# Kernel optimization log

Measured on AMD Instinct MI355X. Metric: run time of the kernel, lower is better.

## Reference

```python
import jax, jax.numpy as jnp
import numpy as np

DS = 8  # downsample_factor


def learned_upflow(flow, mask, ds=DS):
    """Convex-combination upsampling, faithful to Model.learned_upflow.

    flow: (n, 2, h, w)   coarse flow at 1/ds resolution
    mask: (n, 9*ds*ds, h, w)  raw (pre-softmax) convex weights
    returns: (n, 2, ds*h, ds*w)
    """
    n, _, h, w = flow.shape
    # mask.view(n, 1, 9, ds, ds, h, w); softmax over the 9 neighbor taps
    m = mask.reshape(n, 1, 9, ds, ds, h, w)
    m = jax.nn.softmax(m, axis=2)

    # F.unfold(ds*flow, [3,3], padding=1) -> 3x3 neighborhoods, row-major
    # kernel order (dy outer, dx inner), channel-major — matches the
    # subsequent view(n, 2, 9, 1, 1, h, w).
    fp = jnp.pad(ds * flow, ((0, 0), (0, 0), (1, 1), (1, 1)))
    patches = jnp.stack(
        [fp[:, :, dy:dy + h, dx:dx + w] for dy in range(3) for dx in range(3)],
        axis=2,
    )  # (n, 2, 9, h, w)

    up = jnp.sum(m * patches[:, :, :, None, None, :, :], axis=2)  # (n,2,ds,ds,h,w)
    # permute(0,1,4,2,5,3) then reshape -> (n, 2, ds*h, ds*w)
    up = up.transpose(0, 1, 4, 2, 5, 3)
    return up.reshape(n, 2, ds * h, ds * w)


def setup_inputs() -> dict:
    key = jax.random.key(0)
    k1, k2 = jax.random.split(key)
    n, h, w = 4, 136, 240
    flow = jax.random.normal(k1, (n, 2, h, w), dtype=jnp.float32)
    mask = jax.random.normal(k2, (n, 9 * DS * DS, h, w), dtype=jnp.float32)
    return {"flow": flow, "mask": mask}


def reference(flow, mask):
    return learned_upflow(flow, mask)
```

## Files before the change

kernel.cpp:

```cpp
#include <hip/hip_runtime.h>

#define HH 136
#define WW 240
#define HW (HH * WW)
#define DS 8
#define OW (DS * WW)
#define OH (DS * HH)
#define CROWS 12
#define NCH 6

typedef float vf4 __attribute__((ext_vector_type(4)));

__device__ __forceinline__ void gload_lds16(const float* g, float* l) {
  __builtin_amdgcn_global_load_lds(
      (const __attribute__((address_space(1))) void*)g,
      (__attribute__((address_space(3))) void*)l, 16, 0, 0);
}

__global__ __launch_bounds__(256, 7) void upflow_kernel(
    const float* __restrict__ flow,
    const float* __restrict__ mask,
    float* __restrict__ out) {
  __shared__ float lm[2][CROWS][WW];

  int h = blockIdx.x;
  int ni = blockIdx.y;
  int i = ni & 7;
  int n = ni >> 3;
  int tid = threadIdx.x;
  int wid = tid >> 6, lane = tid & 63;
  int px = tid;
  bool stager = lane < 60;

  const float* mrow = mask + ((size_t)n * 576 + i * 8) * HW + (size_t)h * WW;

  if (stager) {
#pragma unroll
    for (int t = 0; t < 3; ++t) {
      int rr = wid + 4 * t;
      gload_lds16(mrow + (size_t)((rr >> 3) * 64 + (rr & 7)) * HW + lane * 4,
                  &lm[0][rr][0]);
    }
  }

  float f0[9], f1[9];
  if (px < WW) {
    const float* fb0 = flow + (size_t)(n * 2 + 0) * HW;
    const float* fb1 = flow + (size_t)(n * 2 + 1) * HW;
#pragma unroll
    for (int dy = 0; dy < 3; ++dy) {
      int hh = h + dy - 1;
      bool rok = (hh >= 0) && (hh < HH);
#pragma unroll
      for (int dx = 0; dx < 3; ++dx) {
        int k = dy * 3 + dx;
        int cc = px + dx - 1;
        bool ok = rok && (cc >= 0) && (cc < WW);
        int idx = hh * WW + cc;
        f0[k] = ok ? 8.0f * fb0[idx] : 0.0f;
        f1[k] = ok ? 8.0f * fb1[idx] : 0.0f;
      }
    }
  }

  const float L2E = 1.4426950408889634f;
  float sj[8], d0j[8], d1j[8];
#pragma unroll
  for (int j = 0; j < 8; ++j) { sj[j] = 0.f; d0j[j] = 0.f; d1j[j] = 0.f; }

#pragma unroll
  for (int c = 0; c < NCH; ++c) {
    if (c + 1 < NCH) {
      if (stager) {
#pragma unroll
        for (int t = 0; t < 3; ++t) {
          int rr = wid + 4 * t;
          int g = (c + 1) * CROWS + rr;
          gload_lds16(
              mrow + (size_t)((g >> 3) * 64 + (g & 7)) * HW + lane * 4,
              &lm[(c + 1) & 1][rr][0]);
        }
      }
      asm volatile("s_waitcnt vmcnt(3)" ::: "memory");
    } else {
      asm volatile("s_waitcnt vmcnt(0)" ::: "memory");
    }
    __builtin_amdgcn_s_barrier();
    asm volatile("" ::: "memory");

    if (px < WW) {
#pragma unroll
      for (int rr = 0; rr < CROWS; ++rr) {
        const int g = c * CROWS + rr;
        const int k = g >> 3, j = g & 7;
        float e = exp2f(lm[c & 1][rr][px] * L2E);
        sj[j] += e;
        d0j[j] += e * f0[k];
        d1j[j] += e * f1[k];
      }
    }

    if (c + 1 < NCH) {
      asm volatile("" ::: "memory");
      __builtin_amdgcn_s_barrier();
      asm volatile("" ::: "memory");
    }
  }

  if (px < WW) {
    size_t ob0 =
        ((size_t)(n * 2 + 0) * OH + (size_t)(h * 8 + i)) * (size_t)OW + px * 8;
    size_t ob1 = ob0 + (size_t)OH * OW;
    float r0 = 1.0f / sj[0], r1 = 1.0f / sj[1], r2 = 1.0f / sj[2],
          r3 = 1.0f / sj[3], r4 = 1.0f / sj[4], r5 = 1.0f / sj[5],
          r6 = 1.0f / sj[6], r7 = 1.0f / sj[7];
    vf4 a = {d0j[0] * r0, d0j[1] * r1, d0j[2] * r2, d0j[3] * r3};
    vf4 b = {d0j[4] * r4, d0j[5] * r5, d0j[6] * r6, d0j[7] * r7};
    vf4 c = {d1j[0] * r0, d1j[1] * r1, d1j[2] * r2, d1j[3] * r3};
    vf4 d = {d1j[4] * r4, d1j[5] * r5, d1j[6] * r6, d1j[7] * r7};
    *(vf4*)(out + ob0) = a;
    *(vf4*)(out + ob0 + 4) = b;
    *(vf4*)(out + ob1) = c;
    *(vf4*)(out + ob1 + 4) = d;
  }
}

extern "C" void kernel_launch(void* const* d_in, const int* in_sizes, int n_in,
                              void* d_out, int out_size, void* d_ws, size_t ws_size,
                              hipStream_t stream) {
  const float* flow = (const float*)d_in[0];
  const float* mask = (const float*)d_in[1];
  float* out = (float*)d_out;
  dim3 grid(HH, 32);
  upflow_kernel<<<grid, 256, 0, stream>>>(flow, mask, out);
}
```

Baseline: 74.66 us.

## Use per-wave private LDS triple buffering and drop block barriers

Each wave now stages only the 60-pixel slice of mask rows it consumes into its own LDS region, so no cross-wave s_barrier is needed. Staging uses 15 lanes issuing 16-byte direct-to-LDS loads, with chunks of 9 rows over 8 chunks, triple buffered and prefetched two chunks ahead using vmcnt waits. Occupancy bound drops from 7 to 6 to make room for the larger buffering. The cost is fewer lanes issuing loads, more outstanding loads per lane, and reliance on exact vmcnt counts being correct.

```diff
diff --git a/kernel.cpp b/kernel.cpp
--- a/kernel.cpp
+++ b/kernel.cpp
@@ -6,8 +6,9 @@
 #define DS 8
 #define OW (DS * WW)
 #define OH (DS * HH)
-#define CROWS 12
-#define NCH 6
+#define CROWS 9
+#define NCH 8
+#define NBUF 3
 
 typedef float vf4 __attribute__((ext_vector_type(4)));
 
@@ -17,34 +18,25 @@
       (__attribute__((address_space(3))) void*)l, 16, 0, 0);
 }
 
-__global__ __launch_bounds__(256, 7) void upflow_kernel(
+__global__ __launch_bounds__(256, 6) void upflow_kernel(
     const float* __restrict__ flow,
     const float* __restrict__ mask,
     float* __restrict__ out) {
-  __shared__ float lm[2][CROWS][WW];
+  __shared__ float lm[4][NBUF][CROWS][60];
 
   int h = blockIdx.x;
   int ni = blockIdx.y;
   int i = ni & 7;
   int n = ni >> 3;
   int tid = threadIdx.x;
-  int wid = tid >> 6, lane = tid & 63;
-  int px = tid;
-  bool stager = lane < 60;
+  int w = tid >> 6, lane = tid & 63;
+  int px = w * 60 + lane;
 
-  const float* mrow = mask + ((size_t)n * 576 + i * 8) * HW + (size_t)h * WW;
-
-  if (stager) {
-#pragma unroll
-    for (int t = 0; t < 3; ++t) {
-      int rr = wid + 4 * t;
-      gload_lds16(mrow + (size_t)((rr >> 3) * 64 + (rr & 7)) * HW + lane * 4,
-                  &lm[0][rr][0]);
-    }
-  }
+  const float* mrow =
+      mask + ((size_t)n * 576 + i * 8) * HW + (size_t)h * WW + w * 60;
 
   float f0[9], f1[9];
-  if (px < WW) {
+  if (lane < 60) {
     const float* fb0 = flow + (size_t)(n * 2 + 0) * HW;
     const float* fb1 = flow + (size_t)(n * 2 + 1) * HW;
 #pragma unroll
@@ -63,6 +55,20 @@
     }
   }
 
+  if (lane < 15) {
+#pragma unroll
+    for (int rr = 0; rr < CROWS; ++rr) {
+      gload_lds16(mrow + (size_t)((rr >> 3) * 64 + (rr & 7)) * HW + lane * 4,
+                  &lm[w][0][rr][0]);
+    }
+#pragma unroll
+    for (int rr = 0; rr < CROWS; ++rr) {
+      int g = CROWS + rr;
+      gload_lds16(mrow + (size_t)((g >> 3) * 64 + (g & 7)) * HW + lane * 4,
+                  &lm[w][1][rr][0]);
+    }
+  }
+
   const float L2E = 1.4426950408889634f;
   float sj[8], d0j[8], d1j[8];
 #pragma unroll
@@ -70,44 +76,36 @@
 
 #pragma unroll
   for (int c = 0; c < NCH; ++c) {
-    if (c + 1 < NCH) {
-      if (stager) {
+    if (c + 2 < NCH) {
+      if (lane < 15) {
 #pragma unroll
-        for (int t = 0; t < 3; ++t) {
-          int rr = wid + 4 * t;
-          int g = (c + 1) * CROWS + rr;
+        for (int rr = 0; rr < CROWS; ++rr) {
+          int g = (c + 2) * CROWS + rr;
           gload_lds16(
               mrow + (size_t)((g >> 3) * 64 + (g & 7)) * HW + lane * 4,
-              &lm[(c + 1) & 1][rr][0]);
+              &lm[w][(c + 2) % NBUF][rr][0]);
         }
       }
-      asm volatile("s_waitcnt vmcnt(3)" ::: "memory");
+      asm volatile("s_waitcnt vmcnt(18)" ::: "memory");
+    } else if (c + 2 == NCH) {
+      asm volatile("s_waitcnt vmcnt(9)" ::: "memory");
     } else {
       asm volatile("s_waitcnt vmcnt(0)" ::: "memory");
     }
-    __builtin_amdgcn_s_barrier();
-    asm volatile("" ::: "memory");
-
-    if (px < WW) {
+    if (lane < 60) {
 #pragma unroll
       for (int rr = 0; rr < CROWS; ++rr) {
         const int g = c * CROWS + rr;
         const int k = g >> 3, j = g & 7;
-        float e = exp2f(lm[c & 1][rr][px] * L2E);
+        float e = exp2f(lm[w][c % NBUF][rr][lane] * L2E);
         sj[j] += e;
         d0j[j] += e * f0[k];
         d1j[j] += e * f1[k];
       }
     }
-
-    if (c + 1 < NCH) {
-      asm volatile("" ::: "memory");
-      __builtin_amdgcn_s_barrier();
-      asm volatile("" ::: "memory");
-    }
   }
 
-  if (px < WW) {
+  if (lane < 60) {
     size_t ob0 =
         ((size_t)(n * 2 + 0) * OH + (size_t)(h * 8 + i)) * (size_t)OW + px * 8;
     size_t ob1 = ob0 + (size_t)OH * OW;
```

New measurement: 87.08 us. +16.6%, slower.

## Triple-buffer mask staging with prefetch distance two and tap-aligned chunks

Applied to the files above, without the earlier changes.

Switches LDS staging of mask rows from two buffers of 12 rows to three buffers of 8 rows, where each chunk is exactly one 3x3 tap. Loads for chunk c+2 are issued while chunk c is processed, with matching vmcnt waits. The aim is to keep more global-to-LDS loads in flight so memory latency is hidden. It also simplifies the inner loop to a single flow value per chunk. It adds more barrier iterations (9 instead of 6), and LDS usage stays about the same.

```diff
diff --git a/kernel.cpp b/kernel.cpp
--- a/kernel.cpp
+++ b/kernel.cpp
@@ -6,8 +6,9 @@
 #define DS 8
 #define OW (DS * WW)
 #define OH (DS * HH)
-#define CROWS 12
-#define NCH 6
+#define CROWS 8
+#define NCH 9
+#define NBUF 3
 
 typedef float vf4 __attribute__((ext_vector_type(4)));
 
@@ -21,27 +22,15 @@
     const float* __restrict__ flow,
     const float* __restrict__ mask,
     float* __restrict__ out) {
-  __shared__ float lm[2][CROWS][WW];
+  __shared__ float lm[NBUF][CROWS][WW];
 
   int h = blockIdx.x;
   int ni = blockIdx.y;
   int i = ni & 7;
   int n = ni >> 3;
   int tid = threadIdx.x;
-  int wid = tid >> 6, lane = tid & 63;
+  int w = tid >> 6, lane = tid & 63;
   int px = tid;
-  bool stager = lane < 60;
-
-  const float* mrow = mask + ((size_t)n * 576 + i * 8) * HW + (size_t)h * WW;
-
-  if (stager) {
-#pragma unroll
-    for (int t = 0; t < 3; ++t) {
-      int rr = wid + 4 * t;
-      gload_lds16(mrow + (size_t)((rr >> 3) * 64 + (rr & 7)) * HW + lane * 4,
-                  &lm[0][rr][0]);
-    }
-  }
 
   float f0[9], f1[9];
   if (px < WW) {
@@ -63,6 +52,21 @@
     }
   }
 
+  const float* mrow = mask + ((size_t)n * 576 + i * 8) * HW + (size_t)h * WW;
+
+  if (lane < 60) {
+#pragma unroll
+    for (int t = 0; t < 2; ++t) {
+      int j = 2 * w + t;
+      gload_lds16(mrow + (size_t)(0 * 64 + j) * HW + lane * 4, &lm[0][j][0]);
+    }
+#pragma unroll
+    for (int t = 0; t < 2; ++t) {
+      int j = 2 * w + t;
+      gload_lds16(mrow + (size_t)(1 * 64 + j) * HW + lane * 4, &lm[1][j][0]);
+    }
+  }
+
   const float L2E = 1.4426950408889634f;
   float sj[8], d0j[8], d1j[8];
 #pragma unroll
@@ -70,18 +74,18 @@
 
 #pragma unroll
   for (int c = 0; c < NCH; ++c) {
-    if (c + 1 < NCH) {
-      if (stager) {
+    if (c + 2 < NCH) {
+      if (lane < 60) {
 #pragma unroll
-        for (int t = 0; t < 3; ++t) {
-          int rr = wid + 4 * t;
-          int g = (c + 1) * CROWS + rr;
-          gload_lds16(
-              mrow + (size_t)((g >> 3) * 64 + (g & 7)) * HW + lane * 4,
-              &lm[(c + 1) & 1][rr][0]);
+        for (int t = 0; t < 2; ++t) {
+          int j = 2 * w + t;
+          gload_lds16(mrow + (size_t)((c + 2) * 64 + j) * HW + lane * 4,
+                      &lm[(c + 2) % NBUF][j][0]);
         }
       }
-      asm volatile("s_waitcnt vmcnt(3)" ::: "memory");
+      asm volatile("s_waitcnt vmcnt(4)" ::: "memory");
+    } else if (c + 2 == NCH) {
+      asm volatile("s_waitcnt vmcnt(2)" ::: "memory");
     } else {
       asm volatile("s_waitcnt vmcnt(0)" ::: "memory");
     }
@@ -89,14 +93,13 @@
     asm volatile("" ::: "memory");
 
     if (px < WW) {
+      const float fc0 = f0[c], fc1 = f1[c];
 #pragma unroll
-      for (int rr = 0; rr < CROWS; ++rr) {
-        const int g = c * CROWS + rr;
-        const int k = g >> 3, j = g & 7;
-        float e = exp2f(lm[c & 1][rr][px] * L2E);
+      for (int j = 0; j < 8; ++j) {
+        float e = exp2f(lm[c % NBUF][j][px] * L2E);
         sj[j] += e;
-        d0j[j] += e * f0[k];
-        d1j[j] += e * f1[k];
+        d0j[j] += e * fc0;
+        d1j[j] += e * fc1;
       }
     }
 
```

After: 75.67 us. Within noise of the previous version (+1.4%).
